# Performance work log

Hardware: AMD Instinct MI355X
Metric: run time of the kernel (lower is better)

The kernel has to match this reference:

```python
import jax, jax.numpy as jnp
import numpy as np

# NFFT config (matches torch NFFT(N=(256,256), m=4, sigma=2.0))
N = (256, 256)          # output Fourier grid
n = (512, 512)          # oversampled grid (2*(int(sigma*N)//2))
m = 4                   # window half-width -> (2m)^2 = 64 taps per point
B, C, M = 2, 2, 200000  # batch, channels, nonuniform points
SIGMA = tuple(n[i] / N[i] for i in range(2))  # KaiserBesselWindow sigma = n/N


def kb_phi(k):
    """Kaiser-Bessel window phi(k), k: (..., 2). Matches KaiserBesselWindow.forward."""
    nv = jnp.asarray(n, dtype=k.dtype)
    b = (2.0 - 1.0 / jnp.asarray(SIGMA, dtype=k.dtype)) * jnp.pi
    t = m * m - (nv * k) ** 2
    safe = t > 0
    arg = jnp.sqrt(jnp.where(safe, t, 1.0))
    out = jnp.where(safe, jnp.sinh(b * arg) / (arg * jnp.pi), 0.0)  # nan_to_num(...,0) equiv.
    return jnp.prod(out, axis=-1)


def kb_phi_hat():
    """Fourier coefficients of the window on the N-grid (KaiserBesselWindow.ft)."""
    grids = jnp.meshgrid(*[jnp.arange(-(N[i] // 2), N[i] // 2, dtype=jnp.float32)
                           for i in range(2)], indexing='ij')
    inds = jnp.stack(grids, axis=-1)                                 # (N1,N2,2)
    nv = jnp.asarray(n, jnp.float32)
    b = (2.0 - 1.0 / jnp.asarray(SIGMA, jnp.float32)) * jnp.pi
    ft = jnp.i0(m * jnp.sqrt(b ** 2 - (2.0 * jnp.pi * inds / nv) ** 2))
    return jnp.prod(ft, axis=-1)                                     # (N1,N2)


def setup_inputs() -> dict:
    key = jax.random.key(0)
    k1, k2, k3 = jax.random.split(key, 3)
    x = jax.random.uniform(k1, (B, 1, M, 2), dtype=jnp.float32) - 0.5  # points in [-1/2,1/2)
    f_hat_real = jax.random.normal(k2, (B, C, N[0], N[1]), dtype=jnp.float32)
    f_hat_imag = jax.random.normal(k3, (B, C, N[0], N[1]), dtype=jnp.float32)
    return {"x": x, "f_hat_real": f_hat_real, "f_hat_imag": f_hat_imag}


def reference(x, f_hat_real, f_hat_imag):
    f_hat = f_hat_real + 1j * f_hat_imag                              # (B,C,N1,N2) complex64
    # deconvolve by window Fourier coefficients
    g_hat = f_hat / kb_phi_hat()
    # zero-pad to oversampled grid n
    cut = [(n[i] - N[i]) // 2 for i in range(2)]
    g_hat = jnp.pad(g_hat, ((0, 0), (0, 0), (cut[0], cut[0]), (cut[1], cut[1])))
    ax = (-2, -1)
    g = jnp.fft.ifftshift(jnp.fft.fft2(jnp.fft.fftshift(g_hat, ax), norm='backward'), ax)
    # windowed gather (sparse_convolution): (2m)^2 taps per nonuniform point
    r = jnp.arange(2 * m, dtype=jnp.int32)
    off = jnp.stack(jnp.meshgrid(r, r, indexing='ij'), axis=-1).reshape(-1, 2)  # (64,2)
    nv = jnp.asarray(n, jnp.float32)
    base = jnp.ceil(x * nv).astype(jnp.int32) - m                     # (B,1,M,2)
    inds = base[None] + off[:, None, None, None, :]                   # (64,B,1,M,2)
    w = kb_phi(x[None] - inds.astype(jnp.float32) / nv)               # (64,B,1,M)
    half = jnp.asarray([n[0] // 2, n[1] // 2], jnp.int32)
    nn = jnp.asarray(n, jnp.int32)
    im = (inds + half) % nn                                           # wrap onto grid
    g2 = jnp.transpose(g, (0, 2, 3, 1))                               # (B,n1,n2,C)
    bidx = jnp.arange(B, dtype=jnp.int32)[None, :, None, None]
    gl = g2[bidx, im[..., 0], im[..., 1]]                             # (64,B,1,M,C)
    f = jnp.sum(gl * w[..., None].astype(gl.dtype), axis=0)           # (B,1,M,C)
    return jnp.transpose(f[:, 0], (0, 2, 1))                          # (B,C,M) complex64
```

## Files before the change

kernel.cpp:

```cpp
#include <hip/hip_runtime.h>
#include <math.h>


#define NGRID 512
#define NSMALL 256
#define MW 4
#define BB 2
#define CC 2
#define MPTS 200000
#define PLANE (BB * CC * MPTS)
#define LPAD4 513
#define GROWS_B 131072
#define GCOLS_OFF 262144
#define GCOLS_B 262144

__device__ __forceinline__ float nfft29781_i0_large(float z) {
    float inv = 1.0f / z;
    float p = 1.0f + inv * (0.125f + inv * (0.0703125f
              + inv * (0.0732421875f + inv * 0.112152099609375f)));
    return expf(z) * rsqrtf(2.0f * (float)M_PI * z) * p;
}

__device__ __forceinline__ int nfft29781_brev9(int v) {
    return (int)(__brev((unsigned)v) >> 23);
}

__device__ __forceinline__ unsigned nfft29781_bf16pack(float a, float b) {
    unsigned ua = __float_as_uint(a);
    ua += 0x7FFFu + ((ua >> 16) & 1u);
    unsigned ub = __float_as_uint(b);
    ub += 0x7FFFu + ((ub >> 16) & 1u);
    return (ua >> 16) | (ub & 0xFFFF0000u);
}

__device__ __forceinline__ float4 nfft29781_unpk(uint2 g) {
    return make_float4(__uint_as_float(g.x << 16),
                       __uint_as_float(g.x & 0xFFFF0000u),
                       __uint_as_float(g.y << 16),
                       __uint_as_float(g.y & 0xFFFF0000u));
}

__device__ __forceinline__ void nfft29781_fft512_c2(float4* s, int tid) {
    #pragma unroll
    for (int st = 0; st < 9; ++st) {
        int half = 1 << st;
        int pos = tid & (half - 1);
        int i0 = ((tid >> st) << (st + 1)) + pos;
        int i1 = i0 + half;
        float ang = -(float)M_PI * (float)pos / (float)half;
        float sn, cs;
        __sincosf(ang, &sn, &cs);
        float4 a = s[i0];
        float4 b = s[i1];
        float4 tw;
        tw.x = b.x * cs - b.y * sn;  tw.y = b.x * sn + b.y * cs;
        tw.z = b.z * cs - b.w * sn;  tw.w = b.z * sn + b.w * cs;
        s[i0] = make_float4(a.x + tw.x, a.y + tw.y, a.z + tw.z, a.w + tw.w);
        s[i1] = make_float4(a.x - tw.x, a.y - tw.y, a.z - tw.z, a.w - tw.w);
        __syncthreads();
    }
}

__global__ __launch_bounds__(256) void nfft29781_rows3(const float* __restrict__ fr,
                                                       const float* __restrict__ fi,
                                                       uint2* __restrict__ Grows) {
    __shared__ float4 s[NGRID];
    int tid = threadIdx.x;
    int b   = blockIdx.x >> 8;
    int a1  = blockIdx.x & 255;

    const float bcon  = 1.5f * (float)M_PI;
    const float scale = 2.0f * (float)M_PI / (float)NGRID;
    float k1 = (float)(a1 - 128) * scale;
    float p1 = nfft29781_i0_large((float)MW * sqrtf(bcon * bcon - k1 * k1));

    int a2 = tid ^ 128;
    float k2 = (float)(a2 - 128) * scale;
    float p2 = nfft29781_i0_large((float)MW * sqrtf(bcon * bcon - k2 * k2));
    float invp = 1.0f / (p1 * p2);

    size_t s0 = ((size_t)(b * CC + 0) * NSMALL + a1) * NSMALL + a2;
    size_t s1 = ((size_t)(b * CC + 1) * NSMALL + a1) * NSMALL + a2;
    float4 v = make_float4(fr[s0] * invp, fi[s0] * invp,
                           fr[s1] * invp, fi[s1] * invp);

    int j2v = (tid < 128) ? tid : tid + 256;
    int j2z = (tid < 128) ? tid + 256 : tid;
    s[nfft29781_brev9(j2v)] = v;
    s[nfft29781_brev9(j2z)] = make_float4(0.0f, 0.0f, 0.0f, 0.0f);
    __syncthreads();

    nfft29781_fft512_c2(s, tid);

    int q = a1 ^ 128;
    uint2* Gr = Grows + ((size_t)b * NSMALL + q) * NGRID;
    float4 v0 = s[tid], v1 = s[tid + 256];
    uint2 pk0, pk1;
    pk0.x = nfft29781_bf16pack(v0.x, v0.y);  pk0.y = nfft29781_bf16pack(v0.z, v0.w);
    pk1.x = nfft29781_bf16pack(v1.x, v1.y);  pk1.y = nfft29781_bf16pack(v1.z, v1.w);
    Gr[tid]       = pk0;
    Gr[tid + 256] = pk1;
}

__global__ __launch_bounds__(256) void nfft29781_cols3(const uint2* __restrict__ Grows,
                                                       uint2* __restrict__ Gcols) {
    __shared__ float4 s[4 * LPAD4];
    int tid  = threadIdx.x;
    int b    = blockIdx.x >> 7;
    int col0 = (blockIdx.x & 127) << 2;
    const uint2* Gr = Grows + (size_t)b * GROWS_B;

    #pragma unroll
    for (int it = 0; it < 4; ++it) {
        int e  = it * 256 + tid;
        int cp = e & 3;
        int q  = e >> 2;
        int r  = (q < 128) ? q : q + 256;
        s[cp * LPAD4 + nfft29781_brev9(r)] =
            nfft29781_unpk(Gr[(size_t)q * NGRID + col0 + cp]);
    }
    #pragma unroll
    for (int it = 0; it < 4; ++it) {
        int e  = it * 256 + tid;
        int cp = e & 3;
        int q  = e >> 2;
        s[cp * LPAD4 + nfft29781_brev9(q + 128)] = make_float4(0.0f, 0.0f, 0.0f, 0.0f);
    }
    __syncthreads();

    int c = tid & 3;
    int w = tid >> 2;
    float4* sc = s + c * LPAD4;
    for (int st = 0; st < 9; ++st) {
        int half = 1 << st;
        #pragma unroll
        for (int k = 0; k < 4; ++k) {
            int bf  = w + (k << 6);
            int pos = bf & (half - 1);
            int i0  = ((bf >> st) << (st + 1)) + pos;
            int i1  = i0 + half;
            float ang = -(float)M_PI * (float)pos / (float)half;
            float sn, cs;
            __sincosf(ang, &sn, &cs);
            float4 a = sc[i0];
            float4 bb = sc[i1];
            float4 tw;
            tw.x = bb.x * cs - bb.y * sn;  tw.y = bb.x * sn + bb.y * cs;
            tw.z = bb.z * cs - bb.w * sn;  tw.w = bb.z * sn + bb.w * cs;
            sc[i0] = make_float4(a.x + tw.x, a.y + tw.y, a.z + tw.z, a.w + tw.w);
            sc[i1] = make_float4(a.x - tw.x, a.y - tw.y, a.z - tw.z, a.w - tw.w);
        }
        __syncthreads();
    }

    uint2* Gc = Gcols + (size_t)b * GCOLS_B;
    #pragma unroll
    for (int it = 0; it < 8; ++it) {
        int e  = it * 256 + tid;
        int cp = e & 3;
        int r  = e >> 2;
        float4 v = s[cp * LPAD4 + r];
        uint2 pk;
        pk.x = nfft29781_bf16pack(v.x, v.y);
        pk.y = nfft29781_bf16pack(v.z, v.w);
        Gc[(size_t)r * NGRID + col0 + cp] = pk;
    }
}

__global__ __launch_bounds__(256) void nfft29781_gather_x2(const float* __restrict__ x,
                                                           const uint2* __restrict__ Gcols,
                                                           float* __restrict__ out,
                                                           int out_elems) {
    int t  = blockIdx.x * blockDim.x + threadIdx.x;
    int j  = t & 7;
    int g2 = t >> 3;
    int pp0 = g2 * 2;
    if (pp0 >= BB * MPTS) return;
    int pp1 = pp0 + 1;

    const float bw = 1.5f * (float)M_PI;
    const float invpi = 1.0f / (float)M_PI;

    int b0  = (pp0 >= MPTS) ? 1 : 0;
    float u00 = x[(size_t)pp0 * 2 + 0] * (float)NGRID;
    float u01 = x[(size_t)pp0 * 2 + 1] * (float)NGRID;
    float c00 = ceilf(u00), c01 = ceilf(u01);
    int base00 = (int)c00 - MW, base01 = (int)c01 - MW;
    float d00 = c00 - u00, d01 = c01 - u01;
    float w0a, w1a;
    {
        float nk = (float)(MW - j) - d00;
        float tt = (float)(MW * MW) - nk * nk;
        w0a = 0.0f;
        if (tt > 0.0f) { float a = sqrtf(tt); float e = expf(bw * a);
                         w0a = (e - 1.0f / e) * 0.5f * invpi / a; }
        nk = (float)(MW - j) - d01;
        tt = (float)(MW * MW) - nk * nk;
        w1a = 0.0f;
        if (tt > 0.0f) { float a = sqrtf(tt); float e = expf(bw * a);
                         w1a = (e - 1.0f / e) * 0.5f * invpi / a; }
    }

    int b1  = (pp1 >= MPTS) ? 1 : 0;
    float u10 = x[(size_t)pp1 * 2 + 0] * (float)NGRID;
    float u11 = x[(size_t)pp1 * 2 + 1] * (float)NGRID;
    float c10 = ceilf(u10), c11 = ceilf(u11);
    int base10 = (int)c10 - MW, base11 = (int)c11 - MW;
    float d10 = c10 - u10, d11 = c11 - u11;
    float w0b, w1b;
    {
        float nk = (float)(MW - j) - d10;
        float tt = (float)(MW * MW) - nk * nk;
        w0b = 0.0f;
        if (tt > 0.0f) { float a = sqrtf(tt); float e = expf(bw * a);
                         w0b = (e - 1.0f / e) * 0.5f * invpi / a; }
        nk = (float)(MW - j) - d11;
        tt = (float)(MW * MW) - nk * nk;
        w1b = 0.0f;
        if (tt > 0.0f) { float a = sqrtf(tt); float e = expf(bw * a);
                         w1b = (e - 1.0f / e) * 0.5f * invpi / a; }
    }

    const uint2* Ga = Gcols + (size_t)b0 * GCOLS_B;
    const uint2* Gb = Gcols + (size_t)b1 * GCOLS_B;
    int cixa = (base01 + j) & (NGRID - 1);
    int cixb = (base11 + j) & (NGRID - 1);
    int lanebase = (threadIdx.x & 63) & ~7;

    float A0 = 0.0f, A1 = 0.0f, A2 = 0.0f, A3 = 0.0f;
    float B0 = 0.0f, B1 = 0.0f, B2 = 0.0f, B3 = 0.0f;
    #pragma unroll
    for (int i = 0; i < 8; ++i) {
        float wa = __shfl(w0a, lanebase + i, 64);
        float wb = __shfl(w0b, lanebase + i, 64);
        uint2 ga = Ga[(size_t)((((base00 + i) & (NGRID - 1)) << 9) + cixa)];
        uint2 gb = Gb[(size_t)((((base10 + i) & (NGRID - 1)) << 9) + cixb)];
        float4 ua = nfft29781_unpk(ga);
        float4 ub = nfft29781_unpk(gb);
        A0 += wa * ua.x;  A1 += wa * ua.y;  A2 += wa * ua.z;  A3 += wa * ua.w;
        B0 += wb * ub.x;  B1 += wb * ub.y;  B2 += wb * ub.z;  B3 += wb * ub.w;
    }
    A0 *= w1a;  A1 *= w1a;  A2 *= w1a;  A3 *= w1a;
    B0 *= w1b;  B1 *= w1b;  B2 *= w1b;  B3 *= w1b;

    #pragma unroll
    for (int msk = 1; msk < 8; msk <<= 1) {
        A0 += __shfl_xor(A0, msk, 64);  A1 += __shfl_xor(A1, msk, 64);
        A2 += __shfl_xor(A2, msk, 64);  A3 += __shfl_xor(A3, msk, 64);
        B0 += __shfl_xor(B0, msk, 64);  B1 += __shfl_xor(B1, msk, 64);
        B2 += __shfl_xor(B2, msk, 64);  B3 += __shfl_xor(B3, msk, 64);
    }

    if (j == 0) {
        int pt0 = pp0 - b0 * MPTS;
        int pt1 = pp1 - b1 * MPTS;
        size_t o00 = (size_t)(b0 * CC) * MPTS + pt0;
        size_t o01 = o00 + MPTS;
        size_t o10 = (size_t)(b1 * CC) * MPTS + pt1;
        size_t o11 = o10 + MPTS;
        if (o00 < (size_t)out_elems)         out[o00]         = A0;
        if (PLANE + o00 < (size_t)out_elems) out[PLANE + o00] = A1;
        if (o01 < (size_t)out_elems)         out[o01]         = A2;
        if (PLANE + o01 < (size_t)out_elems) out[PLANE + o01] = A3;
        if (o10 < (size_t)out_elems)         out[o10]         = B0;
        if (PLANE + o10 < (size_t)out_elems) out[PLANE + o10] = B1;
        if (o11 < (size_t)out_elems)         out[o11]         = B2;
        if (PLANE + o11 < (size_t)out_elems) out[PLANE + o11] = B3;
    }
}

extern "C" void kernel_launch(void* const* d_in, const int* in_sizes, int n_in,
                              void* d_out, int out_size, void* d_ws, size_t ws_size,
                              hipStream_t stream) {
    (void)in_sizes; (void)n_in;
    const float* x  = (const float*)d_in[0];
    const float* fr = (const float*)d_in[1];
    const float* fi = (const float*)d_in[2];
    float* out  = (float*)d_out;
    uint2* Grows = (uint2*)d_ws;
    uint2* Gcols = (uint2*)d_ws + GCOLS_OFF;

    if (ws_size < (size_t)8 * 1024 * 1024) return;

    nfft29781_rows3<<<BB * NSMALL, 256, 0, stream>>>(fr, fi, Grows);
    nfft29781_cols3<<<BB * (NGRID / 4), 256, 0, stream>>>(Grows, Gcols);
    int gthreads = (BB * MPTS / 2) * 8;
    nfft29781_gather_x2<<<(gthreads + 255) / 256, 256, 0, stream>>>(
        x, Gcols, out, out_size);
}
```

Measured before the change: 99.67 us.

## Gather with four lanes per point using DPP broadcasts and quad reductions

The gather kernel is restructured so each point uses four lanes instead of eight, with each lane handling two column taps, replacing one group of eight lanes that processed two points at once. Weight broadcasts and the final reduction use DPP quad permutes instead of ds_bpermute shuffles, which avoids LDS-path cross-lane traffic. Each lane now issues two loads per row and computes four window weights. Thread count stays the same, but there is more per-lane work and fewer reduction steps.

```diff
diff --git a/kernel.cpp b/kernel.cpp
--- a/kernel.cpp
+++ b/kernel.cpp
@@ -167,105 +167,111 @@
     }
 }
 
-__global__ __launch_bounds__(256) void nfft29781_gather_x2(const float* __restrict__ x,
-                                                           const uint2* __restrict__ Gcols,
-                                                           float* __restrict__ out,
-                                                           int out_elems) {
-    int t  = blockIdx.x * blockDim.x + threadIdx.x;
-    int j  = t & 7;
-    int g2 = t >> 3;
-    int pp0 = g2 * 2;
-    if (pp0 >= BB * MPTS) return;
-    int pp1 = pp0 + 1;
-
+template<int CTRL>
+__device__ __forceinline__ float nfft29781_dpp(float v) {
+    return __uint_as_float((unsigned)__builtin_amdgcn_mov_dpp(
+        (int)__float_as_uint(v), CTRL, 0xf, 0xf, true));
+}
+
+template<int I>
+__device__ __forceinline__ float nfft29781_bcast_w0(float w0lo, float w0hi) {
+    constexpr int ctrl = (I >> 1) * 0x55;
+    float src = (I & 1) ? w0hi : w0lo;
+    return nfft29781_dpp<ctrl>(src);
+}
+
+__device__ __forceinline__ float nfft29781_qsum(float v) {
+    v += nfft29781_dpp<0xB1>(v);
+    v += nfft29781_dpp<0x4E>(v);
+    return v;
+}
+
+__device__ __forceinline__ float nfft29781_w(int tap, float d) {
     const float bw = 1.5f * (float)M_PI;
     const float invpi = 1.0f / (float)M_PI;
-
-    int b0  = (pp0 >= MPTS) ? 1 : 0;
-    float u00 = x[(size_t)pp0 * 2 + 0] * (float)NGRID;
-    float u01 = x[(size_t)pp0 * 2 + 1] * (float)NGRID;
-    float c00 = ceilf(u00), c01 = ceilf(u01);
-    int base00 = (int)c00 - MW, base01 = (int)c01 - MW;
-    float d00 = c00 - u00, d01 = c01 - u01;
-    float w0a, w1a;
-    {
-        float nk = (float)(MW - j) - d00;
-        float tt = (float)(MW * MW) - nk * nk;
-        w0a = 0.0f;
-        if (tt > 0.0f) { float a = sqrtf(tt); float e = expf(bw * a);
-                         w0a = (e - 1.0f / e) * 0.5f * invpi / a; }
-        nk = (float)(MW - j) - d01;
-        tt = (float)(MW * MW) - nk * nk;
-        w1a = 0.0f;
-        if (tt > 0.0f) { float a = sqrtf(tt); float e = expf(bw * a);
-                         w1a = (e - 1.0f / e) * 0.5f * invpi / a; }
-    }
-
-    int b1  = (pp1 >= MPTS) ? 1 : 0;
-    float u10 = x[(size_t)pp1 * 2 + 0] * (float)NGRID;
-    float u11 = x[(size_t)pp1 * 2 + 1] * (float)NGRID;
-    float c10 = ceilf(u10), c11 = ceilf(u11);
-    int base10 = (int)c10 - MW, base11 = (int)c11 - MW;
-    float d10 = c10 - u10, d11 = c11 - u11;
-    float w0b, w1b;
-    {
-        float nk = (float)(MW - j) - d10;
-        float tt = (float)(MW * MW) - nk * nk;
-        w0b = 0.0f;
-        if (tt > 0.0f) { float a = sqrtf(tt); float e = expf(bw * a);
-                         w0b = (e - 1.0f / e) * 0.5f * invpi / a; }
-        nk = (float)(MW - j) - d11;
-        tt = (float)(MW * MW) - nk * nk;
-        w1b = 0.0f;
-        if (tt > 0.0f) { float a = sqrtf(tt); float e = expf(bw * a);
-                         w1b = (e - 1.0f / e) * 0.5f * invpi / a; }
-    }
-
-    const uint2* Ga = Gcols + (size_t)b0 * GCOLS_B;
-    const uint2* Gb = Gcols + (size_t)b1 * GCOLS_B;
-    int cixa = (base01 + j) & (NGRID - 1);
-    int cixb = (base11 + j) & (NGRID - 1);
-    int lanebase = (threadIdx.x & 63) & ~7;
-
-    float A0 = 0.0f, A1 = 0.0f, A2 = 0.0f, A3 = 0.0f;
-    float B0 = 0.0f, B1 = 0.0f, B2 = 0.0f, B3 = 0.0f;
-    #pragma unroll
-    for (int i = 0; i < 8; ++i) {
-        float wa = __shfl(w0a, lanebase + i, 64);
-        float wb = __shfl(w0b, lanebase + i, 64);
-        uint2 ga = Ga[(size_t)((((base00 + i) & (NGRID - 1)) << 9) + cixa)];
-        uint2 gb = Gb[(size_t)((((base10 + i) & (NGRID - 1)) << 9) + cixb)];
-        float4 ua = nfft29781_unpk(ga);
-        float4 ub = nfft29781_unpk(gb);
-        A0 += wa * ua.x;  A1 += wa * ua.y;  A2 += wa * ua.z;  A3 += wa * ua.w;
-        B0 += wb * ub.x;  B1 += wb * ub.y;  B2 += wb * ub.z;  B3 += wb * ub.w;
-    }
-    A0 *= w1a;  A1 *= w1a;  A2 *= w1a;  A3 *= w1a;
-    B0 *= w1b;  B1 *= w1b;  B2 *= w1b;  B3 *= w1b;
-
-    #pragma unroll
-    for (int msk = 1; msk < 8; msk <<= 1) {
-        A0 += __shfl_xor(A0, msk, 64);  A1 += __shfl_xor(A1, msk, 64);
-        A2 += __shfl_xor(A2, msk, 64);  A3 += __shfl_xor(A3, msk, 64);
-        B0 += __shfl_xor(B0, msk, 64);  B1 += __shfl_xor(B1, msk, 64);
-        B2 += __shfl_xor(B2, msk, 64);  B3 += __shfl_xor(B3, msk, 64);
-    }
+    float nk = (float)(MW - tap) - d;
+    float tt = (float)(MW * MW) - nk * nk;
+    float wv = 0.0f;
+    if (tt > 0.0f) {
+        float a = sqrtf(tt);
+        float e = expf(bw * a);
+        wv = (e - 1.0f / e) * 0.5f * invpi / a;
+    }
+    return wv;
+}
+
+template<int I>
+__device__ __forceinline__ void nfft29781_step(const uint2* __restrict__ Gi,
+                                               int base0, int cix0, int cix1,
+                                               float w0lo, float w0hi,
+                                               float* a0, float* a1) {
+    float w0i = nfft29781_bcast_w0<I>(w0lo, w0hi);
+    int row = (base0 + I) & (NGRID - 1);
+    const uint2* rp = Gi + ((size_t)row << 9);
+    float4 u0 = nfft29781_unpk(rp[cix0]);
+    float4 u1 = nfft29781_unpk(rp[cix1]);
+    a0[0] += w0i * u0.x;  a0[1] += w0i * u0.y;
+    a0[2] += w0i * u0.z;  a0[3] += w0i * u0.w;
+    a1[0] += w0i * u1.x;  a1[1] += w0i * u1.y;
+    a1[2] += w0i * u1.z;  a1[3] += w0i * u1.w;
+}
+
+__global__ __launch_bounds__(256) void nfft29781_gather_dpp(const float* __restrict__ x,
+                                                            const uint2* __restrict__ Gcols,
+                                                            float* __restrict__ out,
+                                                            int out_elems) {
+    int t  = blockIdx.x * blockDim.x + threadIdx.x;
+    int j  = t & 3;
+    int pp = t >> 2;
+    if (pp >= BB * MPTS) return;
+    int b  = (pp >= MPTS) ? 1 : 0;
+    int pt = pp - b * MPTS;
+
+    float2 xv = ((const float2*)x)[pp];
+    float u0 = xv.x * (float)NGRID;
+    float u1 = xv.y * (float)NGRID;
+    float c0 = ceilf(u0), c1 = ceilf(u1);
+    int base0 = (int)c0 - MW;
+    int base1 = (int)c1 - MW;
+    float d0 = c0 - u0, d1 = c1 - u1;
+
+    int t0 = 2 * j, t1 = 2 * j + 1;
+    float w0lo = nfft29781_w(t0, d0);
+    float w0hi = nfft29781_w(t1, d0);
+    float w1lo = nfft29781_w(t0, d1);
+    float w1hi = nfft29781_w(t1, d1);
+
+    const uint2* Gi = Gcols + (size_t)b * GCOLS_B;
+    int cix0 = (base1 + t0) & (NGRID - 1);
+    int cix1 = (base1 + t1) & (NGRID - 1);
+
+    float a0[4] = {0.f, 0.f, 0.f, 0.f};
+    float a1[4] = {0.f, 0.f, 0.f, 0.f};
+    nfft29781_step<0>(Gi, base0, cix0, cix1, w0lo, w0hi, a0, a1);
+    nfft29781_step<1>(Gi, base0, cix0, cix1, w0lo, w0hi, a0, a1);
+    nfft29781_step<2>(Gi, base0, cix0, cix1, w0lo, w0hi, a0, a1);
+    nfft29781_step<3>(Gi, base0, cix0, cix1, w0lo, w0hi, a0, a1);
+    nfft29781_step<4>(Gi, base0, cix0, cix1, w0lo, w0hi, a0, a1);
+    nfft29781_step<5>(Gi, base0, cix0, cix1, w0lo, w0hi, a0, a1);
+    nfft29781_step<6>(Gi, base0, cix0, cix1, w0lo, w0hi, a0, a1);
+    nfft29781_step<7>(Gi, base0, cix0, cix1, w0lo, w0hi, a0, a1);
+
+    float r0 = w1lo * a0[0] + w1hi * a1[0];
+    float r1 = w1lo * a0[1] + w1hi * a1[1];
+    float r2 = w1lo * a0[2] + w1hi * a1[2];
+    float r3 = w1lo * a0[3] + w1hi * a1[3];
+    r0 = nfft29781_qsum(r0);
+    r1 = nfft29781_qsum(r1);
+    r2 = nfft29781_qsum(r2);
+    r3 = nfft29781_qsum(r3);
 
     if (j == 0) {
-        int pt0 = pp0 - b0 * MPTS;
-        int pt1 = pp1 - b1 * MPTS;
-        size_t o00 = (size_t)(b0 * CC) * MPTS + pt0;
-        size_t o01 = o00 + MPTS;
-        size_t o10 = (size_t)(b1 * CC) * MPTS + pt1;
-        size_t o11 = o10 + MPTS;
-        if (o00 < (size_t)out_elems)         out[o00]         = A0;
-        if (PLANE + o00 < (size_t)out_elems) out[PLANE + o00] = A1;
-        if (o01 < (size_t)out_elems)         out[o01]         = A2;
-        if (PLANE + o01 < (size_t)out_elems) out[PLANE + o01] = A3;
-        if (o10 < (size_t)out_elems)         out[o10]         = B0;
-        if (PLANE + o10 < (size_t)out_elems) out[PLANE + o10] = B1;
-        if (o11 < (size_t)out_elems)         out[o11]         = B2;
-        if (PLANE + o11 < (size_t)out_elems) out[PLANE + o11] = B3;
+        size_t o0 = (size_t)(b * CC) * MPTS + pt;
+        size_t o1 = o0 + MPTS;
+        if (o0 < (size_t)out_elems)         out[o0]         = r0;
+        if (PLANE + o0 < (size_t)out_elems) out[PLANE + o0] = r1;
+        if (o1 < (size_t)out_elems)         out[o1]         = r2;
+        if (PLANE + o1 < (size_t)out_elems) out[PLANE + o1] = r3;
     }
 }
 
@@ -284,7 +290,7 @@
 
     nfft29781_rows3<<<BB * NSMALL, 256, 0, stream>>>(fr, fi, Grows);
     nfft29781_cols3<<<BB * (NGRID / 4), 256, 0, stream>>>(Grows, Gcols);
-    int gthreads = (BB * MPTS / 2) * 8;
-    nfft29781_gather_x2<<<(gthreads + 255) / 256, 256, 0, stream>>>(
+    int gthreads = BB * MPTS * 4;
+    nfft29781_gather_dpp<<<(gthreads + 255) / 256, 256, 0, stream>>>(
         x, Gcols, out, out_size);
 }
```

Measured after the change: 101.6 us. No clear change (+2.0%).
